# Optimization experiments

Measured on AMD Instinct MI355X. Metric: run time of the kernel, lower is better.

## Reference

```python
import jax, jax.numpy as jnp
import numpy as np

B, L, R, D = 4, 1024, 4, 1024   # batch, seq, expansion rate, model dim
HEADS, HD, FF = 16, 64, 4096
EPS = 1e-6


def _static_alpha(layer_id):
    a0 = np.zeros((R, 1), np.float32)
    a0[layer_id % R, 0] = 1.0
    return jnp.asarray(np.concatenate([a0, np.eye(R, dtype=np.float32)], axis=1))  # [R, R+1]


def setup_inputs() -> dict:
    key = jax.random.key(0)
    ks = jax.random.split(key, 12)
    w = lambda k, shape, s=0.02: (jax.random.normal(k, shape, jnp.float32) * s)
    return {
        "H": jax.random.normal(ks[0], (B, L, R, D), jnp.float32),
        # attention hyper-connection (layer_id*2 = 0)
        "hc1_norm_w": jnp.ones((D,), jnp.float32),
        "hc1_alpha_fn": w(ks[1], (D, R + 1), 0.01),
        "hc1_beta_fn": w(ks[2], (D,), 0.01),
        "hc1_a_scale": jnp.full((1,), 0.01, jnp.float32),
        "hc1_b_scale": jnp.full((1,), 0.01, jnp.float32),
        "hc1_s_alpha": _static_alpha(0),
        "hc1_s_beta": jnp.ones((R,), jnp.float32),
        # attention
        "attn_norm_w": jnp.ones((D,), jnp.float32),
        "qkv_w": w(ks[3], (3 * D, D)),
        "out_w": w(ks[4], (D, D)),
        # ffn hyper-connection (layer_id*2+1 = 1)
        "hc2_norm_w": jnp.ones((D,), jnp.float32),
        "hc2_alpha_fn": w(ks[5], (D, R + 1), 0.01),
        "hc2_beta_fn": w(ks[6], (D,), 0.01),
        "hc2_a_scale": jnp.full((1,), 0.01, jnp.float32),
        "hc2_b_scale": jnp.full((1,), 0.01, jnp.float32),
        "hc2_s_alpha": _static_alpha(1),
        "hc2_s_beta": jnp.ones((R,), jnp.float32),
        # ffn
        "ffn_norm_w": jnp.ones((D,), jnp.float32),
        "fc1_w": w(ks[7], (FF, D)),
        "fc2_w": w(ks[8], (D, FF)),
    }


def _rms(x, weight):
    norm = jnp.sqrt(jnp.mean(x * x, axis=-1, keepdims=True))
    return weight * x / (norm + EPS)


def _width(Hm, norm_w, alpha_fn, beta_fn, a_scale, b_scale, s_alpha, s_beta):
    nh = _rms(Hm, norm_w)                                      # [B,L,R,D]
    alpha = jnp.tanh(jnp.einsum('blnd,dk->blnk', nh, alpha_fn)) * a_scale + s_alpha  # [B,L,R,R+1]
    beta = jnp.tanh(jnp.einsum('blnd,d->bln', nh, beta_fn)) * b_scale + s_beta       # [B,L,R]
    mix = jnp.einsum('blnk,blnd->blkd', alpha, Hm)             # [B,L,R+1,D]
    return mix, beta


def _depth(mix, out, beta):
    return beta[..., None] * out[:, :, None, :] + mix[..., 1:, :]


def _attention(x, qkv_w, out_w):
    b, l, d = x.shape
    qkv = (x @ qkv_w.T).reshape(b, l, 3, HEADS, HD)
    q, k, v = (jnp.moveaxis(qkv, 2, 0)[i].transpose(0, 2, 1, 3) for i in range(3))  # [B,H,L,HD]
    scores = jnp.einsum('bhqd,bhkd->bhqk', q, k) * (HD ** -0.5)
    causal = jnp.tril(jnp.ones((l, l), bool))
    scores = jnp.where(causal, scores, jnp.float32(-jnp.inf))
    attn = jax.nn.softmax(scores, axis=-1)
    out = jnp.einsum('bhqk,bhkd->bhqd', attn, v).transpose(0, 2, 1, 3).reshape(b, l, d)
    return out @ out_w.T


def reference(H, hc1_norm_w, hc1_alpha_fn, hc1_beta_fn, hc1_a_scale, hc1_b_scale,
              hc1_s_alpha, hc1_s_beta, attn_norm_w, qkv_w, out_w,
              hc2_norm_w, hc2_alpha_fn, hc2_beta_fn, hc2_a_scale, hc2_b_scale,
              hc2_s_alpha, hc2_s_beta, ffn_norm_w, fc1_w, fc2_w):
    # attention block
    mix, beta = _width(H, hc1_norm_w, hc1_alpha_fn, hc1_beta_fn,
                       hc1_a_scale, hc1_b_scale, hc1_s_alpha, hc1_s_beta)
    h = _rms(mix[..., 0, :], attn_norm_w)
    h = _attention(h, qkv_w, out_w)
    H = _depth(mix, h, beta)
    # ffn block
    mix, beta = _width(H, hc2_norm_w, hc2_alpha_fn, hc2_beta_fn,
                       hc2_a_scale, hc2_b_scale, hc2_s_alpha, hc2_s_beta)
    h = _rms(mix[..., 0, :], ffn_norm_w)
    h = (jax.nn.gelu(h @ fc1_w.T, approximate=False)) @ fc2_w.T
    H = _depth(mix, h, beta)
    return H
```

## Files before the change

### kernel.cpp

```cpp
#include <hip/hip_runtime.h>
#include <math.h>

#define BB 4
#define LL 1024
#define RR 4
#define DD 1024
#define NHEADS 16
#define HDIM 64
#define FFD 4096
#define EPSV 1e-6f

typedef short s16x8 __attribute__((ext_vector_type(8)));
typedef float f32x4 __attribute__((ext_vector_type(4)));
typedef unsigned short u16;

__device__ inline unsigned short f2bf(float x) {
  unsigned u = __builtin_bit_cast(unsigned, x);
  unsigned r = (u + 0x7fffu + ((u >> 16) & 1u)) >> 16;
  return (unsigned short)r;
}
__device__ inline float bf2f(u16 x) {
  return __builtin_bit_cast(float, (unsigned)x << 16);
}

__device__ inline float wred_xor(float v) {
#pragma unroll
  for (int off = 1; off < 64; off <<= 1) v += __shfl_xor(v, off);
  return v;
}

__device__ inline void gload_lds16(const u16* g, u16* l) {
  __builtin_amdgcn_global_load_lds(
      (const __attribute__((address_space(1))) unsigned int*)g,
      (__attribute__((address_space(3))) unsigned int*)l, 16, 0, 0);
}

__global__ __launch_bounds__(256) void cvt4_kernel(
    const float* __restrict__ s0, const float* __restrict__ s1,
    const float* __restrict__ s2, const float* __restrict__ s3,
    u16* __restrict__ d0, u16* __restrict__ d1,
    u16* __restrict__ d2, u16* __restrict__ d3) {
  const int n0 = 786432, n1 = 262144, n2 = 1048576, n3 = 1048576;
  const int total = n0 + n1 + n2 + n3;
  for (int i = blockIdx.x * 256 + threadIdx.x; i < total; i += gridDim.x * 256) {
    const float4* src; ushort4* dst; int j;
    if (i < n0)                { src = (const float4*)s0; dst = (ushort4*)d0; j = i; }
    else if (i < n0 + n1)      { src = (const float4*)s1; dst = (ushort4*)d1; j = i - n0; }
    else if (i < n0 + n1 + n2) { src = (const float4*)s2; dst = (ushort4*)d2; j = i - n0 - n1; }
    else                       { src = (const float4*)s3; dst = (ushort4*)d3; j = i - n0 - n1 - n2; }
    float4 v = src[j];
    ushort4 o;
    o.x = f2bf(v.x); o.y = f2bf(v.y); o.z = f2bf(v.z); o.w = f2bf(v.w);
    dst[j] = o;
  }
}

template<int NP>
__global__ __launch_bounds__(256) void width_kernel(
    const float* __restrict__ Hin,
    const u16* __restrict__ mixrest_in,
    const float* __restrict__ beta_in,
    const u16* __restrict__ pp,
    const float* __restrict__ hc_norm_w,
    const float* __restrict__ alpha_fn,
    const float* __restrict__ beta_fn,
    const float* __restrict__ a_scale,
    const float* __restrict__ b_scale,
    const float* __restrict__ s_alpha,
    const float* __restrict__ s_beta,
    const float* __restrict__ post_norm_w,
    u16* __restrict__ mixrest_out,
    float* __restrict__ beta_out,
    u16* __restrict__ x_out)
{
  const size_t MN = (size_t)4096 * 1024;
  const int l = threadIdx.x & 63, w = threadIdx.x >> 6;
  const int bl = blockIdx.x * 4 + w;
  const int d0 = l << 2;

  float4 h[4][4];
  if (NP > 0) {
    float be[4];
#pragma unroll
    for (int n = 0; n < 4; ++n) be[n] = beta_in[bl * 4 + n];
#pragma unroll
    for (int i = 0; i < 4; ++i) {
      const int d = i * 256 + d0;
      float4 s; s.x = 0.f; s.y = 0.f; s.z = 0.f; s.w = 0.f;
#pragma unroll
      for (int p = 0; p < (NP > 0 ? NP : 1); ++p) {
        ushort4 v = *(const ushort4*)&pp[p * MN + (size_t)bl * 1024 + d];
        s.x += bf2f(v.x); s.y += bf2f(v.y); s.z += bf2f(v.z); s.w += bf2f(v.w);
      }
#pragma unroll
      for (int n = 0; n < 4; ++n) {
        ushort4 mr = *(const ushort4*)&mixrest_in[(size_t)bl * 4096 + n * 1024 + d];
        h[n][i].x = be[n] * s.x + bf2f(mr.x);
        h[n][i].y = be[n] * s.y + bf2f(mr.y);
        h[n][i].z = be[n] * s.z + bf2f(mr.z);
        h[n][i].w = be[n] * s.w + bf2f(mr.w);
      }
    }
  } else {
#pragma unroll
    for (int i = 0; i < 4; ++i) {
      const int d = i * 256 + d0;
#pragma unroll
      for (int n = 0; n < 4; ++n)
        h[n][i] = *(const float4*)&Hin[(size_t)bl * 4096 + n * 1024 + d];
    }
  }

  float inv[4];
#pragma unroll
  for (int n = 0; n < 4; ++n) {
    float a = 0.f;
#pragma unroll
    for (int i = 0; i < 4; ++i)
      a += h[n][i].x * h[n][i].x + h[n][i].y * h[n][i].y +
           h[n][i].z * h[n][i].z + h[n][i].w * h[n][i].w;
    a = wred_xor(a);
    inv[n] = 1.f / (sqrtf(a * (1.f / 1024.f)) + EPSV);
  }

  float dots[4][6];
#pragma unroll
  for (int n = 0; n < 4; ++n)
#pragma unroll
    for (int k = 0; k < 6; ++k) dots[n][k] = 0.f;
#pragma unroll
  for (int i = 0; i < 4; ++i) {
    const int d = i * 256 + d0;
    float4 nw = *(const float4*)&hc_norm_w[d];
    float4 bfv4 = *(const float4*)&beta_fn[d];
    float4 A0 = *(const float4*)&alpha_fn[d * 5];
    float4 A1 = *(const float4*)&alpha_fn[d * 5 + 4];
    float4 A2 = *(const float4*)&alpha_fn[d * 5 + 8];
    float4 A3 = *(const float4*)&alpha_fn[d * 5 + 12];
    float4 A4 = *(const float4*)&alpha_fn[d * 5 + 16];
    const float af[4][5] = {
        {A0.x, A0.y, A0.z, A0.w, A1.x},
        {A1.y, A1.z, A1.w, A2.x, A2.y},
        {A2.z, A2.w, A3.x, A3.y, A3.z},
        {A3.w, A4.x, A4.y, A4.z, A4.w}};
    const float nwv[4] = {nw.x, nw.y, nw.z, nw.w};
    const float bfl[4] = {bfv4.x, bfv4.y, bfv4.z, bfv4.w};
#pragma unroll
    for (int j = 0; j < 4; ++j) {
      const float wj = nwv[j];
#pragma unroll
      for (int n = 0; n < 4; ++n) {
        const float hw = (j == 0 ? h[n][i].x : j == 1 ? h[n][i].y : j == 2 ? h[n][i].z : h[n][i].w) * wj;
        dots[n][0] += hw * af[j][0];
        dots[n][1] += hw * af[j][1];
        dots[n][2] += hw * af[j][2];
        dots[n][3] += hw * af[j][3];
        dots[n][4] += hw * af[j][4];
        dots[n][5] += hw * bfl[j];
      }
    }
  }
  const float as = a_scale[0], bs = b_scale[0];
  float alpha[4][5], betav[4];
#pragma unroll
  for (int n = 0; n < 4; ++n) {
#pragma unroll
    for (int k = 0; k < 5; ++k) {
      float r = wred_xor(dots[n][k]);
      alpha[n][k] = tanhf(r * inv[n]) * as + s_alpha[n * 5 + k];
    }
    float rb = wred_xor(dots[n][5]);
    betav[n] = tanhf(rb * inv[n]) * bs + s_beta[n];
  }
  if (l == 0) {
#pragma unroll
    for (int n = 0; n < 4; ++n) beta_out[bl * 4 + n] = betav[n];
  }

  float4 mix0[4];
#pragma unroll
  for (int i = 0; i < 4; ++i) {
    const int d = i * 256 + d0;
#pragma unroll
    for (int k = 0; k < 5; ++k) {
      const float c0 = alpha[0][k], c1 = alpha[1][k], c2 = alpha[2][k], c3 = alpha[3][k];
      float4 mv;
      mv.x = c0 * h[0][i].x + c1 * h[1][i].x + c2 * h[2][i].x + c3 * h[3][i].x;
      mv.y = c0 * h[0][i].y + c1 * h[1][i].y + c2 * h[2][i].y + c3 * h[3][i].y;
      mv.z = c0 * h[0][i].z + c1 * h[1][i].z + c2 * h[2][i].z + c3 * h[3][i].z;
      mv.w = c0 * h[0][i].w + c1 * h[1][i].w + c2 * h[2][i].w + c3 * h[3][i].w;
      if (k == 0) {
        mix0[i] = mv;
      } else {
        ushort4 ov;
        ov.x = f2bf(mv.x); ov.y = f2bf(mv.y); ov.z = f2bf(mv.z); ov.w = f2bf(mv.w);
        *(ushort4*)&mixrest_out[(size_t)bl * 4096 + (size_t)(k - 1) * 1024 + d] = ov;
      }
    }
  }

  float a0s = 0.f;
#pragma unroll
  for (int i = 0; i < 4; ++i)
    a0s += mix0[i].x * mix0[i].x + mix0[i].y * mix0[i].y +
           mix0[i].z * mix0[i].z + mix0[i].w * mix0[i].w;
  a0s = wred_xor(a0s);
  const float iv0 = 1.f / (sqrtf(a0s * (1.f / 1024.f)) + EPSV);
#pragma unroll
  for (int i = 0; i < 4; ++i) {
    const int d = i * 256 + d0;
    float4 pw = *(const float4*)&post_norm_w[d];
    ushort4 ov;
    ov.x = f2bf(pw.x * mix0[i].x * iv0);
    ov.y = f2bf(pw.y * mix0[i].y * iv0);
    ov.z = f2bf(pw.z * mix0[i].z * iv0);
    ov.w = f2bf(pw.w * mix0[i].w * iv0);
    *(ushort4*)&x_out[(size_t)bl * 1024 + d] = ov;
  }
}

template<int EPI, int SPLIT>
__global__ __launch_bounds__(256, 4) void gemm_bt_kernel(
    const u16* __restrict__ A, const u16* __restrict__ W,
    u16* __restrict__ Cb, u16* __restrict__ Vt,
    int M, int N, int K)
{
  __shared__ __align__(16) u16 LDSb[2][2][128 * 32];
  const int tn = N >> 7, tm = M >> 7;
  int bid = blockIdx.x;
  const int nwg = gridDim.x;
  if ((nwg & 7) == 0) bid = (bid & 7) * (nwg >> 3) + (bid >> 3);
  const int ts = tm * tn;
  const int sK = bid / ts;
  const int tb = bid - sK * ts;
  const int bm = tb / tn, bn = tb % tn;
  const int Kc = K / SPLIT;
  const int kbeg = sK * Kc;

  const int t = threadIdx.x, l = t & 63, w = t >> 6;
  const int wr = w >> 1, wc = w & 1;
  const int m0 = bm << 7, n0 = bn << 7;
  const int ssc = (((l & 3) ^ ((l >> 3) & 3)) << 3);
  const int srA = m0 + (w << 5) + (l >> 2);
  const int srB = n0 + (w << 5) + (l >> 2);
  const int ldso = (w << 10);
  const int fr = l & 15, g4 = l >> 4;
  const int fc8 = ((g4 ^ ((l >> 1) & 3)) << 3);

  f32x4 acc[4][4];
#pragma unroll
  for (int i = 0; i < 4; ++i)
#pragma unroll
    for (int j = 0; j < 4; ++j)
#pragma unroll
      for (int e = 0; e < 4; ++e) acc[i][j][e] = 0.f;

  const u16* pa0 = A + (size_t)srA * K + kbeg + ssc;
  const u16* pa1 = A + (size_t)(srA + 16) * K + kbeg + ssc;
  const u16* pb0 = W + (size_t)srB * K + kbeg + ssc;
  const u16* pb1 = W + (size_t)(srB + 16) * K + kbeg + ssc;

#define STAGE(buf, koff)                                   \
  do {                                                     \
    gload_lds16(pa0 + (koff), &LDSb[buf][0][ldso]);        \
    gload_lds16(pa1 + (koff), &LDSb[buf][0][ldso + 512]);  \
    gload_lds16(pb0 + (koff), &LDSb[buf][1][ldso]);        \
    gload_lds16(pb1 + (koff), &LDSb[buf][1][ldso + 512]);  \
  } while (0)

  const int nt = Kc >> 5;
  STAGE(0, 0);
  int cur = 0;
  for (int kt = 0; kt < nt; ++kt) {
    if (kt + 1 < nt) {
      STAGE(cur ^ 1, (kt + 1) << 5);
      asm volatile("s_waitcnt vmcnt(4)" ::: "memory");
    } else {
      asm volatile("s_waitcnt vmcnt(0)" ::: "memory");
    }
    __builtin_amdgcn_s_barrier();
    __builtin_amdgcn_sched_barrier(0);
    s16x8 af[4], bfr[4];
#pragma unroll
    for (int m = 0; m < 4; ++m)
      af[m] = *(const s16x8*)(&LDSb[cur][0][(wr * 64 + m * 16 + fr) * 32 + fc8]);
#pragma unroll
    for (int n = 0; n < 4; ++n)
      bfr[n] = *(const s16x8*)(&LDSb[cur][1][(wc * 64 + n * 16 + fr) * 32 + fc8]);
#pragma unroll
    for (int m = 0; m < 4; ++m)
#pragma unroll
      for (int n = 0; n < 4; ++n)
        acc[m][n] = __builtin_amdgcn_mfma_f32_16x16x32_bf16(af[m], bfr[n], acc[m][n], 0, 0, 0);
    asm volatile("s_waitcnt lgkmcnt(0)" ::: "memory");
    __builtin_amdgcn_sched_barrier(0);
    __builtin_amdgcn_s_barrier();
    cur ^= 1;
  }
#undef STAGE

  if (EPI == 2 && n0 >= 2048) {
    const int rbv = m0 + wr * 64 + (g4 << 2);
    const int cbv = n0 + wc * 64 + fr;
#pragma unroll
    for (int m = 0; m < 4; ++m)
#pragma unroll
      for (int n = 0; n < 4; ++n) {
        int cc = cbv + n * 16 - 2048;
        int hh = cc >> 6, dd = cc & 63;
        int r0 = rbv + m * 16;
        ushort4 ov;
        ov.x = f2bf(acc[m][n][0]); ov.y = f2bf(acc[m][n][1]);
        ov.z = f2bf(acc[m][n][2]); ov.w = f2bf(acc[m][n][3]);
        *(ushort4*)&Vt[((size_t)((r0 >> 10) * 16 + hh) * 64 + dd) * 1024 + (r0 & 1023)] = ov;
      }
    return;
  }

  float* scr = (float*)LDSb;
  const int strideN = (EPI == 2) ? 2048 : N;
  u16* Cout = (SPLIT > 1) ? (Cb + (size_t)sK * M * N) : Cb;
#pragma unroll
  for (int r = 0; r < 2; ++r) {
    __syncthreads();
    if (wr == r) {
#pragma unroll
      for (int m = 0; m < 4; ++m)
#pragma unroll
        for (int n = 0; n < 4; ++n)
#pragma unroll
          for (int j = 0; j < 4; ++j) {
            int lr = m * 16 + (g4 << 2) + j;
            int col = wc * 64 + n * 16 + fr;
            scr[lr * 128 + (col ^ ((((lr >> 2) & 7)) << 3))] = acc[m][n][j];
          }
    }
    __syncthreads();
#pragma unroll
    for (int it = 0; it < 4; ++it) {
      int lr = it * 16 + (t >> 4);
      int key8 = ((lr >> 2) & 7) << 3;
      int lc = (t & 15) << 3;
      int cb0 = (lc ^ key8);
      f32x4 v0 = *(const f32x4*)&scr[lr * 128 + cb0];
      f32x4 v1 = *(const f32x4*)&scr[lr * 128 + cb0 + 4];
      float vv[8] = {v0[0], v0[1], v0[2], v0[3], v1[0], v1[1], v1[2], v1[3]};
      s16x8 ov;
#pragma unroll
      for (int c = 0; c < 8; ++c) {
        float v = vv[c];
        if (EPI == 1) v = 0.5f * v * (1.f + erff(v * 0.70710678118f));
        ov[c] = (short)f2bf(v);
      }
      size_t gr = (size_t)(m0 + r * 64 + lr);
      *(s16x8*)&Cout[gr * strideN + n0 + lc] = ov;
    }
  }
}

__global__ __launch_bounds__(256) void attn_mfma_kernel(
    const u16* __restrict__ qk, const u16* __restrict__ Vt, u16* __restrict__ out)
{
  const int id = blockIdx.x;
  const int hb = id & 63, qt0 = id >> 6;
  const int b = hb >> 4, h = hb & 15;
  const int qt = (h & 1) ? (15 - qt0) : qt0;
  const int t = threadIdx.x, l = t & 63, w = t >> 6;
  const int q0 = qt << 6;
  __shared__ __align__(16) u16 Ks[2][64 * 64];
  __shared__ __align__(16) u16 Vs[2][64 * 64];
  __shared__ __align__(16) u16 Ps[4][16 * 64];

  const int fr = l & 15;
  const int fg = (l >> 4) << 3;
  const int fswz = (fr & 7) << 3;

  const int qrow = q0 + w * 16 + fr;
  const size_t qbase = (size_t)(b * 1024 + qrow) * 2048 + h * 64 + fg;
  const s16x8 aq0 = *(const s16x8*)(qk + qbase);
  const s16x8 aq1 = *(const s16x8*)(qk + qbase + 32);

  f32x4 acc_o[4];
#pragma unroll
  for (int i = 0; i < 4; ++i)
#pragma unroll
    for (int e = 0; e < 4; ++e) acc_o[i][e] = 0.f;
  float m_i[4] = {-INFINITY, -INFINITY, -INFINITY, -INFINITY};
  float l_i[4] = {0.f, 0.f, 0.f, 0.f};

  const int sr = (w << 3) + (l >> 3);
  const int scs = (((l & 7) ^ ((l >> 3) & 7)) << 3);
  const u16* ksrc = qk + (size_t)(b * 1024 + sr) * 2048 + 1024 + h * 64 + scs;
  const u16* vsrc = Vt + ((size_t)((b * 16 + h) * 64 + sr)) * 1024 + scs;
  const int ldst = (w << 9);

#define ASTAGE(buf, kb_)                                                     \
  do {                                                                       \
    gload_lds16(ksrc + (size_t)(kb_) * 2048, &Ks[buf][ldst]);                \
    gload_lds16(ksrc + (size_t)((kb_) + 32) * 2048, &Ks[buf][2048 + ldst]);  \
    gload_lds16(vsrc + (kb_), &Vs[buf][ldst]);                               \
    gload_lds16(vsrc + (kb_) + 32 * 1024, &Vs[buf][2048 + ldst]);            \
  } while (0)

  const int qrow_c = q0 + w * 16 + ((l >> 4) << 2);
  u16* Psw = &Ps[w][0];
  const int nkt = qt + 1;

  ASTAGE(0, 0);
  int cur = 0;
  for (int kt = 0; kt < nkt; ++kt) {
    const int kb = kt << 6;
    if (kt + 1 < nkt) {
      ASTAGE(cur ^ 1, (kt + 1) << 6);
      asm volatile("s_waitcnt vmcnt(4)" ::: "memory");
    } else {
      asm volatile("s_waitcnt vmcnt(0)" ::: "memory");
    }
    __builtin_amdgcn_s_barrier();
    __builtin_amdgcn_sched_barrier(0);

    f32x4 s[4];
#pragma unroll
    for (int n = 0; n < 4; ++n) {
#pragma unroll
      for (int e = 0; e < 4; ++e) s[n][e] = 0.f;
      s16x8 bk0 = *(const s16x8*)(&Ks[cur][(n * 16 + fr) * 64 + (fg ^ fswz)]);
      s16x8 bk1 = *(const s16x8*)(&Ks[cur][(n * 16 + fr) * 64 + ((32 + fg) ^ fswz)]);
      s[n] = __builtin_amdgcn_mfma_f32_16x16x32_bf16(aq0, bk0, s[n], 0, 0, 0);
      s[n] = __builtin_amdgcn_mfma_f32_16x16x32_bf16(aq1, bk1, s[n], 0, 0, 0);
    }
#pragma unroll
    for (int n = 0; n < 4; ++n)
#pragma unroll
      for (int e = 0; e < 4; ++e) s[n][e] *= 0.125f;
    if (kt == nkt - 1 && kb == q0) {
#pragma unroll
      for (int n = 0; n < 4; ++n) {
        int kc = kb + n * 16 + fr;
#pragma unroll
        for (int r = 0; r < 4; ++r)
          if (kc > qrow_c + r) s[n][r] = -INFINITY;
      }
    }

    float rm[4], fac[4];
#pragma unroll
    for (int r = 0; r < 4; ++r)
      rm[r] = fmaxf(fmaxf(s[0][r], s[1][r]), fmaxf(s[2][r], s[3][r]));
#pragma unroll
    for (int off = 1; off < 16; off <<= 1)
#pragma unroll
      for (int r = 0; r < 4; ++r) rm[r] = fmaxf(rm[r], __shfl_xor(rm[r], off));
#pragma unroll
    for (int r = 0; r < 4; ++r) {
      float mn = fmaxf(m_i[r], rm[r]);
      fac[r] = __expf(m_i[r] - mn);
      m_i[r] = mn;
    }
    float rs[4] = {0.f, 0.f, 0.f, 0.f};
    float pb[4][4];
#pragma unroll
    for (int n = 0; n < 4; ++n)
#pragma unroll
      for (int r = 0; r < 4; ++r) {
        float pv = __expf(s[n][r] - m_i[r]);
        pb[n][r] = pv;
        rs[r] += pv;
      }
#pragma unroll
    for (int off = 1; off < 16; off <<= 1)
#pragma unroll
      for (int r = 0; r < 4; ++r) rs[r] += __shfl_xor(rs[r], off);
#pragma unroll
    for (int r = 0; r < 4; ++r) l_i[r] = l_i[r] * fac[r] + rs[r];
#pragma unroll
    for (int dt = 0; dt < 4; ++dt)
#pragma unroll
      for (int r = 0; r < 4; ++r) acc_o[dt][r] *= fac[r];

#pragma unroll
    for (int n = 0; n < 4; ++n)
#pragma unroll
      for (int r = 0; r < 4; ++r) {
        int prow = ((l >> 4) << 2) + r;
        Psw[prow * 64 + ((n * 16 + fr) ^ ((prow & 7) << 3))] = f2bf(pb[n][r]);
      }
    asm volatile("s_waitcnt lgkmcnt(0)" ::: "memory");
    __builtin_amdgcn_sched_barrier(0);

    s16x8 pa0 = *(const s16x8*)(Psw + fr * 64 + (fg ^ fswz));
    s16x8 pa1 = *(const s16x8*)(Psw + fr * 64 + ((32 + fg) ^ fswz));
#pragma unroll
    for (int dt = 0; dt < 4; ++dt) {
      s16x8 bv0 = *(const s16x8*)(&Vs[cur][(dt * 16 + fr) * 64 + (fg ^ fswz)]);
      s16x8 bv1 = *(const s16x8*)(&Vs[cur][(dt * 16 + fr) * 64 + ((32 + fg) ^ fswz)]);
      acc_o[dt] = __builtin_amdgcn_mfma_f32_16x16x32_bf16(pa0, bv0, acc_o[dt], 0, 0, 0);
      acc_o[dt] = __builtin_amdgcn_mfma_f32_16x16x32_bf16(pa1, bv1, acc_o[dt], 0, 0, 0);
    }
    asm volatile("s_waitcnt lgkmcnt(0)" ::: "memory");
    __builtin_amdgcn_sched_barrier(0);
    __builtin_amdgcn_s_barrier();
    cur ^= 1;
  }
#undef ASTAGE

  float invl[4];
#pragma unroll
  for (int r = 0; r < 4; ++r) invl[r] = 1.f / l_i[r];
#pragma unroll
  for (int dt = 0; dt < 4; ++dt)
#pragma unroll
    for (int r = 0; r < 4; ++r) {
      size_t idx = (size_t)(b * 1024 + qrow_c + r) * 1024 + h * 64 + dt * 16 + fr;
      out[idx] = f2bf(acc_o[dt][r] * invl[r]);
    }
}

template<int NPART>
__global__ __launch_bounds__(256) void depth2_kernel(
    const u16* __restrict__ parts, const u16* __restrict__ mixrest,
    const float* __restrict__ beta, float* __restrict__ Hout)
{
  const size_t MN = (size_t)4096 * 1024;
  const size_t stride = (size_t)gridDim.x * 256;
  const size_t n8 = (size_t)BB * LL * RR * DD / 8;
  for (size_t i = (size_t)blockIdx.x * 256 + threadIdx.x; i < n8; i += stride) {
    size_t e = i * 8;
    int d = (int)(e & 1023);
    int n = (int)((e >> 10) & 3);
    size_t bl = e >> 12;
    float be = beta[bl * 4 + n];
    float f[8];
#pragma unroll
    for (int j = 0; j < 8; ++j) f[j] = 0.f;
#pragma unroll
    for (int p = 0; p < NPART; ++p) {
      s16x8 v = *(const s16x8*)&parts[p * MN + bl * 1024 + d];
#pragma unroll
      for (int j = 0; j < 8; ++j) f[j] += bf2f((u16)v[j]);
    }
    s16x8 m = *(const s16x8*)&mixrest[e];
    float4 o0, o1;
    o0.x = be * f[0] + bf2f((u16)m[0]); o0.y = be * f[1] + bf2f((u16)m[1]);
    o0.z = be * f[2] + bf2f((u16)m[2]); o0.w = be * f[3] + bf2f((u16)m[3]);
    o1.x = be * f[4] + bf2f((u16)m[4]); o1.y = be * f[5] + bf2f((u16)m[5]);
    o1.z = be * f[6] + bf2f((u16)m[6]); o1.w = be * f[7] + bf2f((u16)m[7]);
    *(float4*)&Hout[e] = o0;
    *(float4*)&Hout[e + 4] = o1;
  }
}

extern "C" void kernel_launch(void* const* d_in, const int* in_sizes, int n_in,
                              void* d_out, int out_size, void* d_ws, size_t ws_size,
                              hipStream_t stream) {
  const float* H       = (const float*)d_in[0];
  const float* hc1_nw  = (const float*)d_in[1];
  const float* hc1_afn = (const float*)d_in[2];
  const float* hc1_bfn = (const float*)d_in[3];
  const float* hc1_as  = (const float*)d_in[4];
  const float* hc1_bs  = (const float*)d_in[5];
  const float* hc1_sa  = (const float*)d_in[6];
  const float* hc1_sb  = (const float*)d_in[7];
  const float* attn_nw = (const float*)d_in[8];
  const float* qkv_w   = (const float*)d_in[9];
  const float* out_w   = (const float*)d_in[10];
  const float* hc2_nw  = (const float*)d_in[11];
  const float* hc2_afn = (const float*)d_in[12];
  const float* hc2_bfn = (const float*)d_in[13];
  const float* hc2_as  = (const float*)d_in[14];
  const float* hc2_bs  = (const float*)d_in[15];
  const float* hc2_sa  = (const float*)d_in[16];
  const float* hc2_sb  = (const float*)d_in[17];
  const float* ffn_nw  = (const float*)d_in[18];
  const float* fc1_w   = (const float*)d_in[19];
  const float* fc2_w   = (const float*)d_in[20];
  float* Hout = (float*)d_out;

  char* wsp = (char*)d_ws;
  size_t off = 0;
  auto carve = [&](size_t bytes) {
    void* p = wsp + off;
    off = (off + bytes + 255) & ~(size_t)255;
    return p;
  };
  const size_t MN = (size_t)4096 * 1024;
  u16* wq_bf   = (u16*)carve((size_t)3072 * 1024 * 2);
  u16* wo_bf   = (u16*)carve((size_t)1024 * 1024 * 2);
  u16* w1_bf   = (u16*)carve((size_t)4096 * 1024 * 2);
  u16* w2_bf   = (u16*)carve((size_t)4096 * 1024 * 2);
  u16* xbf     = (u16*)carve((size_t)4096 * 1024 * 2);
  u16* mixrest = (u16*)carve((size_t)4096 * 4096 * 2);
  float* beta1 = (float*)carve((size_t)16384 * 4);
  float* beta2 = (float*)carve((size_t)16384 * 4);
  char* uregion = (char*)carve((size_t)32 * 1024 * 1024);
  u16* qk_bf   = (u16*)uregion;
  u16* Vt      = (u16*)(uregion + (size_t)16 * 1024 * 1024);
  u16* g1_bf   = (u16*)uregion;
  u16* attn_bf = (u16*)carve((size_t)4096 * 1024 * 2);
  u16* pp      = (u16*)carve((size_t)4 * MN * 2);

  cvt4_kernel<<<2048, 256, 0, stream>>>(qkv_w, out_w, fc1_w, fc2_w, wq_bf, wo_bf, w1_bf, w2_bf);
  width_kernel<0><<<1024, 256, 0, stream>>>(H, nullptr, nullptr, nullptr,
      hc1_nw, hc1_afn, hc1_bfn, hc1_as, hc1_bs, hc1_sa, hc1_sb, attn_nw,
      mixrest, beta1, xbf);
  gemm_bt_kernel<2, 1><<<768, 256, 0, stream>>>(xbf, wq_bf, qk_bf, Vt, 4096, 3072, 1024);
  attn_mfma_kernel<<<1024, 256, 0, stream>>>(qk_bf, Vt, attn_bf);
  gemm_bt_kernel<0, 4><<<1024, 256, 0, stream>>>(attn_bf, wo_bf, pp, nullptr, 4096, 1024, 1024);
  width_kernel<4><<<1024, 256, 0, stream>>>(nullptr, mixrest, beta1, pp,
      hc2_nw, hc2_afn, hc2_bfn, hc2_as, hc2_bs, hc2_sa, hc2_sb, ffn_nw,
      mixrest, beta2, xbf);
  gemm_bt_kernel<1, 1><<<1024, 256, 0, stream>>>(xbf, w1_bf, g1_bf, nullptr, 4096, 4096, 1024);
  gemm_bt_kernel<0, 4><<<1024, 256, 0, stream>>>(g1_bf, w2_bf, pp, nullptr, 4096, 1024, 4096);
  depth2_kernel<4><<<4096, 256, 0, stream>>>(pp, mixrest, beta2, Hout);
}
```

Baseline: 301.2 us.

## Add 256x256-tile 8-wave GEMM kernel for FFN fc1 and fc2

Adds a new GEMM kernel with 256x256 output tiles, 512 threads, double-buffered LDS loads, and a ping-pong interleave of LDS fragment loads with MFMA using barriers and setprio. The two FFN GEMMs (fc1 with GELU, and fc2 with split-K 4) now use it, each with 256 workgroups instead of 1024. The aim is higher arithmetic intensity and data reuse per tile, which cuts global and LDS traffic per flop. The trade-off is fewer workgroups to fill the CUs, which can hurt wave-level load balance, and a large LDS footprint of 128KB.

```diff
diff --git a/kernel.cpp b/kernel.cpp
--- a/kernel.cpp
+++ b/kernel.cpp
@@ -354,6 +354,155 @@
       }
       size_t gr = (size_t)(m0 + r * 64 + lr);
       *(s16x8*)&Cout[gr * strideN + n0 + lc] = ov;
+    }
+  }
+}
+
+template<int EPI, int SPLIT>
+__global__ __launch_bounds__(512, 1) void gemm256_kernel(
+    const u16* __restrict__ A, const u16* __restrict__ W,
+    u16* __restrict__ Cb,
+    int M, int N, int K)
+{
+  __shared__ __align__(16) u16 As[2][256 * 64];
+  __shared__ __align__(16) u16 Bs[2][256 * 64];
+  const int tn = N >> 8, tm = M >> 8;
+  int bid = blockIdx.x;
+  const int nwg = gridDim.x;
+  bid = (bid & 7) * (nwg >> 3) + (bid >> 3);
+  const int ts = tm * tn;
+  const int sK = bid / ts;
+  const int tb = bid - sK * ts;
+  const int bm = tb / tn, bn = tb % tn;
+  const int Kc = K / SPLIT;
+  const int kbeg = sK * Kc;
+
+  const int t = threadIdx.x, l = t & 63, w = t >> 6;
+  const int wr = w >> 2, wc = w & 3;
+  const int m0g = bm << 8, n0g = bn << 8;
+  const int fr = l & 15, g4 = l >> 4;
+
+  const int srow = t >> 3;
+  const int gsc8 = (((t & 7) ^ (srow & 7)) << 3);
+  const u16* pA = A + (size_t)(m0g + srow) * K + kbeg + gsc8;
+  const u16* pB = W + (size_t)(n0g + srow) * K + kbeg + gsc8;
+
+#define STG_A(rb, buf, ko) gload_lds16(pA + (size_t)(rb) * K + (ko), &As[buf][(rb) * 64 + (t << 3)])
+#define STG_B(rb, buf, ko) gload_lds16(pB + (size_t)(rb) * K + (ko), &Bs[buf][(rb) * 64 + (t << 3)])
+#define LDA(dst, mh, kk)                                                                   \
+  {                                                                                        \
+    _Pragma("unroll") for (int j = 0; j < 4; ++j)                                          \
+        dst[j] = *(const s16x8*)(&As[c][(wr * 128 + ((mh)*4 + j) * 16 + fr) * 64 +         \
+                                        ((((kk)*4 + g4) ^ (fr & 7)) << 3)]);               \
+  }
+#define LDB(dst, kk)                                                                       \
+  {                                                                                        \
+    _Pragma("unroll") for (int n = 0; n < 4; ++n)                                          \
+        dst[n] = *(const s16x8*)(&Bs[c][(wc * 64 + n * 16 + fr) * 64 +                     \
+                                        ((((kk)*4 + g4) ^ (fr & 7)) << 3)]);               \
+  }
+#define MM(mh, BF)                                                                         \
+  _Pragma("unroll") for (int j = 0; j < 4; ++j)                                            \
+      _Pragma("unroll") for (int n = 0; n < 4; ++n)                                        \
+          acc[(mh)*4 + j][n] =                                                             \
+              __builtin_amdgcn_mfma_f32_16x16x32_bf16(af[j], BF[n], acc[(mh)*4 + j][n], 0, 0, 0);
+#define LGKM0                                            \
+  asm volatile("s_waitcnt lgkmcnt(0)" ::: "memory");     \
+  __builtin_amdgcn_sched_barrier(0)
+#define BAR                                              \
+  __builtin_amdgcn_s_barrier();                          \
+  __builtin_amdgcn_sched_barrier(0)
+
+  f32x4 acc[8][4];
+#pragma unroll
+  for (int i = 0; i < 8; ++i)
+#pragma unroll
+    for (int j = 0; j < 4; ++j)
+#pragma unroll
+      for (int e = 0; e < 4; ++e) acc[i][j][e] = 0.f;
+
+  const int nt = Kc >> 6;
+  STG_B(0, 0, 0); STG_B(64, 0, 0);
+  STG_B(128, 0, 0); STG_B(192, 0, 0);
+  STG_A(0, 0, 0); STG_A(128, 0, 0);
+  STG_A(64, 0, 0); STG_A(192, 0, 0);
+
+  int c = 0;
+  for (int kt = 0; kt < nt; ++kt) {
+    const bool st = (kt + 1 < nt);
+    const int ko = (kt + 1) << 6;
+    const int nb = c ^ 1;
+    s16x8 af[4], bf0[4], bf1[4];
+    asm volatile("s_waitcnt vmcnt(2)" ::: "memory");
+    BAR;
+    if (st) { STG_B(0, nb, ko); STG_B(64, nb, ko); }
+    LDA(af, 0, 0); LDB(bf0, 0);
+    LGKM0;
+    __builtin_amdgcn_s_setprio(1); MM(0, bf0); __builtin_amdgcn_s_setprio(0);
+    BAR;
+    if (st) { STG_B(128, nb, ko); STG_B(192, nb, ko); }
+    LDA(af, 0, 1); LDB(bf1, 1);
+    LGKM0;
+    __builtin_amdgcn_s_setprio(1); MM(0, bf1); __builtin_amdgcn_s_setprio(0);
+    if (st) asm volatile("s_waitcnt vmcnt(4)" ::: "memory");
+    else    asm volatile("s_waitcnt vmcnt(0)" ::: "memory");
+    BAR;
+    if (st) { STG_A(0, nb, ko); STG_A(128, nb, ko); }
+    LDA(af, 1, 0);
+    LGKM0;
+    __builtin_amdgcn_s_setprio(1); MM(1, bf0); __builtin_amdgcn_s_setprio(0);
+    BAR;
+    if (st) { STG_A(64, nb, ko); STG_A(192, nb, ko); }
+    LDA(af, 1, 1);
+    LGKM0;
+    __builtin_amdgcn_s_setprio(1); MM(1, bf1); __builtin_amdgcn_s_setprio(0);
+    c = nb;
+  }
+#undef STG_A
+#undef STG_B
+#undef LDA
+#undef LDB
+#undef MM
+#undef LGKM0
+#undef BAR
+
+  float* scr = (float*)As;
+  u16* Cout = (SPLIT > 1) ? (Cb + (size_t)sK * M * N) : Cb;
+#pragma unroll
+  for (int rb = 0; rb < 4; ++rb) {
+    __syncthreads();
+    if (wr == (rb >> 1)) {
+      const int mlo = (rb & 1) * 4;
+#pragma unroll
+      for (int mm = 0; mm < 4; ++mm)
+#pragma unroll
+        for (int n = 0; n < 4; ++n)
+#pragma unroll
+          for (int j = 0; j < 4; ++j) {
+            int lr = mm * 16 + (g4 << 2) + j;
+            int col = wc * 64 + n * 16 + fr;
+            scr[lr * 256 + (col ^ (((lr >> 2) & 7) << 3))] = acc[mlo + mm][n][j];
+          }
+    }
+    __syncthreads();
+#pragma unroll
+    for (int it = 0; it < 4; ++it) {
+      int lr = it * 16 + (t >> 5);
+      int key8 = ((lr >> 2) & 7) << 3;
+      int lc = (t & 31) << 3;
+      int cb0 = lc ^ key8;
+      f32x4 v0 = *(const f32x4*)&scr[lr * 256 + cb0];
+      f32x4 v1 = *(const f32x4*)&scr[lr * 256 + cb0 + 4];
+      float vv[8] = {v0[0], v0[1], v0[2], v0[3], v1[0], v1[1], v1[2], v1[3]};
+      s16x8 ov;
+#pragma unroll
+      for (int cc = 0; cc < 8; ++cc) {
+        float v = vv[cc];
+        if (EPI == 1) v = 0.5f * v * (1.f + erff(v * 0.70710678118f));
+        ov[cc] = (short)f2bf(v);
+      }
+      size_t gr = (size_t)(m0g + rb * 64 + lr);
+      *(s16x8*)&Cout[gr * N + n0g + lc] = ov;
     }
   }
 }
@@ -609,7 +758,7 @@
   width_kernel<4><<<1024, 256, 0, stream>>>(nullptr, mixrest, beta1, pp,
       hc2_nw, hc2_afn, hc2_bfn, hc2_as, hc2_bs, hc2_sa, hc2_sb, ffn_nw,
       mixrest, beta2, xbf);
-  gemm_bt_kernel<1, 1><<<1024, 256, 0, stream>>>(xbf, w1_bf, g1_bf, nullptr, 4096, 4096, 1024);
-  gemm_bt_kernel<0, 4><<<1024, 256, 0, stream>>>(g1_bf, w2_bf, pp, nullptr, 4096, 1024, 4096);
+  gemm256_kernel<1, 1><<<256, 512, 0, stream>>>(xbf, w1_bf, g1_bf, 4096, 4096, 1024);
+  gemm256_kernel<0, 4><<<256, 512, 0, stream>>>(g1_bf, w2_bf, pp, 4096, 1024, 4096);
   depth2_kernel<4><<<4096, 256, 0, stream>>>(pp, mixrest, beta2, Hout);
 }
```

After: 328.4 us. +9.0%, slower.
